# Optimization experiments

Hardware: AMD Instinct MI355X
Metric: run time of the kernel (lower is better)

## Reference

```python
import jax, jax.numpy as jnp
import numpy as np

ALPHA = 0.5            # conf['alpha'] hybrid mixing
MAX_TOP_ANT = 50       # conf['max_top_antecedents']
MAX_SPAN_WIDTH = 30


def bucket_distance(d):
    # util.bucket_distance: identity 0..4, then log2 buckets, clipped to [0, 9]
    logspace = jnp.floor(jnp.log2(jnp.maximum(d, 1).astype(jnp.float32))).astype(d.dtype) + 3
    return jnp.clip(jnp.where(d <= 4, d, logspace), 0, 9)


def setup_inputs() -> dict:
    key = jax.random.key(0)
    ks = jax.random.split(key, 16)
    W, D, K, F, H = 4096, 768, 768, 20, 1000
    SPAN = 3 * D                      # span_emb_size = 3 * bert_emb_size
    PAIR = 3 * SPAN + F               # pair_emb_size (use_features only)
    std = 0.02

    mention_doc = jax.random.normal(ks[0], (W, D), jnp.float32)
    mention_doc_one = jax.random.normal(ks[1], (W, D), jnp.float32)
    top_span_starts = jnp.sort(jax.random.randint(ks[2], (K,), 0, W - MAX_SPAN_WIDTH))
    widths = jax.random.randint(ks[3], (K,), 0, MAX_SPAN_WIDTH)
    top_span_ends = jnp.minimum(top_span_starts + widths, W - 1)
    top_span_mention_scores = jax.random.normal(ks[4], (K,), jnp.float32)

    return {
        "mention_doc": mention_doc,
        "mention_doc_one": mention_doc_one,
        "top_span_starts": top_span_starts,
        "top_span_ends": top_span_ends,
        "top_span_mention_scores": top_span_mention_scores,
        # mention_token_attn: Linear(D -> 1)
        "attn_w": jax.random.normal(ks[5], (D,), jnp.float32) * std,
        "attn_b": jnp.zeros((), jnp.float32),
        # coarse_bilinear: Linear(SPAN -> SPAN)
        "coarse_w": jax.random.normal(ks[6], (SPAN, SPAN), jnp.float32) * std,
        "coarse_b": jnp.zeros((SPAN,), jnp.float32),
        # emb_antecedent_distance_prior [10, F] + antecedent_distance_score_ffnn Linear(F -> 1)
        "dist_prior_emb": jax.random.normal(ks[7], (10, F), jnp.float32) * std,
        "dist_w": jax.random.normal(ks[8], (F,), jnp.float32) * std,
        "dist_b": jnp.zeros((), jnp.float32),
        # emb_top_antecedent_distance [10, F]
        "top_dist_emb": jax.random.normal(ks[9], (10, F), jnp.float32) * std,
        # coref_score_ffnn: Linear(PAIR -> H), ReLU, Linear(H -> 1)
        "coref_w1": jax.random.normal(ks[10], (PAIR, H), jnp.float32) * std,
        "coref_b1": jnp.zeros((H,), jnp.float32),
        "coref_w2": jax.random.normal(ks[11], (H,), jnp.float32) * std,
        "coref_b2": jnp.zeros((), jnp.float32),
    }


def reference(mention_doc, mention_doc_one, top_span_starts, top_span_ends,
              top_span_mention_scores, attn_w, attn_b, coarse_w, coarse_b,
              dist_prior_emb, dist_w, dist_b, top_dist_emb,
              coref_w1, coref_b1, coref_w2, coref_b2):
    W = mention_doc.shape[0]
    K = top_span_starts.shape[0]
    C = min(K, MAX_TOP_ANT)
    NEG_INF = jnp.float32(-1e30) * 0 - jnp.inf  # true -inf, matches torch.log(0.)

    # --- span embeddings: start / end / head-attention over hybrid doc ---
    start_emb = mention_doc[top_span_starts]                      # [K, D]
    end_emb = mention_doc[top_span_ends]                          # [K, D]
    hybrid = mention_doc * (1.0 - ALPHA) + mention_doc_one * ALPHA
    token_attn = hybrid @ attn_w + attn_b                         # [W]
    tok = jnp.arange(W)
    span_tok_mask = (tok[None, :] >= top_span_starts[:, None]) & \
                    (tok[None, :] <= top_span_ends[:, None])      # [K, W]
    attn_raw = jnp.where(span_tok_mask, token_attn[None, :], NEG_INF)
    attn_probs = jax.nn.softmax(attn_raw, axis=1)                 # [K, W]
    head_emb = attn_probs @ hybrid                                # [K, D]
    span_emb = jnp.concatenate([start_emb, end_emb, head_emb], axis=1)  # [K, 3D]

    # --- coarse (fast) pairwise scores ---
    rng = jnp.arange(K)
    ant_offsets = rng[:, None] - rng[None, :]                     # [K, K]
    ant_mask = ant_offsets >= 1
    pair_sum = top_span_mention_scores[:, None] + top_span_mention_scores[None, :]
    src = span_emb @ coarse_w + coarse_b                          # coarse_bilinear
    fast = pair_sum + src @ span_emb.T
    fast = jnp.where(ant_mask, fast, NEG_INF)                     # + log(mask)
    dist_score = dist_prior_emb @ dist_w + dist_b                 # [10]
    fast = fast + dist_score[bucket_distance(ant_offsets)]        # distance prior

    # --- top-k antecedent pruning ---
    top_fast, top_idx = jax.lax.top_k(fast, C)                    # [K, C]
    top_ant_offsets = jnp.take_along_axis(ant_offsets, top_idx, axis=1)

    # --- fine-grained pairwise FFNN scoring ---
    dist_emb = top_dist_emb[bucket_distance(top_ant_offsets)]     # [K, C, F]
    ant_emb = span_emb[top_idx]                                   # [K, C, 3D]
    tgt_emb = jnp.broadcast_to(span_emb[:, None, :], ant_emb.shape)
    sim_emb = span_emb[:, None, :] * ant_emb
    pair_emb = jnp.concatenate([tgt_emb, ant_emb, sim_emb, dist_emb], axis=-1)  # [K, C, PAIR]
    h = jax.nn.relu(jnp.einsum('kcp,ph->kch', pair_emb, coref_w1) + coref_b1)
    slow = jnp.einsum('kch,h->kc', h, coref_w2) + coref_b2        # [K, C]
    top_scores = slow + top_fast

    # dummy antecedent (epsilon) column of zeros
    return jnp.concatenate([jnp.zeros((K, 1), top_scores.dtype), top_scores], axis=1)
```

## Files before the change

### kernel.cpp

```cpp
#include <hip/hip_runtime.h>
#include <math.h>

#define WTOK 4096
#define DD   768
#define KK   768
#define SPAN 2304
#define HH   1000
#define CC   50
#define NPAD 1024
#define NBIG 4352

typedef __attribute__((ext_vector_type(8))) short bf16x8;
typedef __attribute__((ext_vector_type(4))) float f32x4;
typedef unsigned short ushort;
typedef unsigned int uint;

__device__ __forceinline__ int bucketd(int d) {
  int l = (d >= 1) ? (31 - __clz(d)) : 0;
  int v = (d <= 4) ? d : (l + 3);
  return min(max(v, 0), 9);
}
__device__ __forceinline__ ushort f2bf(float f) {
  uint u = __float_as_uint(f);
  return (ushort)((u + 0x7fffu + ((u >> 16) & 1u)) >> 16);
}
__device__ __forceinline__ uint pkmul_t(uint a, uint b) {
  float lo = __uint_as_float(a << 16) * __uint_as_float(b << 16);
  float hi = __uint_as_float(a & 0xffff0000u) * __uint_as_float(b & 0xffff0000u);
  return (__float_as_uint(lo) >> 16) | (__float_as_uint(hi) & 0xffff0000u);
}
__device__ __forceinline__ uint4 pkmul4(uint4 a, uint4 b) {
  uint4 r;
  r.x = pkmul_t(a.x, b.x); r.y = pkmul_t(a.y, b.y);
  r.z = pkmul_t(a.z, b.z); r.w = pkmul_t(a.w, b.w);
  return r;
}
__device__ __forceinline__ void dma16(const ushort* g, ushort* l) {
  __builtin_amdgcn_global_load_lds(
      (const __attribute__((address_space(1))) void*)g,
      (__attribute__((address_space(3))) void*)l, 16, 0, 0);
}

#define PB_COARSE 5184
#define PB_W 2304
#define PB_SETUP_BASE (PB_COARSE + 3 * PB_W)
#define PB_SLOW_BASE  (PB_SETUP_BASE + 40)
#define PB_TOTAL      (PB_SLOW_BASE + 150)

__global__ __launch_bounds__(256) void prep_k(
    const float* __restrict__ coarse_w, const float* __restrict__ W1,
    const float* __restrict__ dist_prior, const float* __restrict__ dist_w,
    const float* __restrict__ dist_b, const float* __restrict__ top_dist,
    ushort* __restrict__ BigT, ushort* __restrict__ W1simT,
    float* __restrict__ dist_score, float* __restrict__ Pdist,
    float* __restrict__ slow)
{
  int bid = blockIdx.x;
  int tid = threadIdx.x;
  if (bid >= PB_SLOW_BASE) {
    int t = (bid - PB_SLOW_BASE) * 256 + tid;
    if (t < KK * CC) slow[t] = 0.f;
    return;
  }
  if (bid >= PB_SETUP_BASE) {
    int t = (bid - PB_SETUP_BASE) * 256 + tid;
    if (t < 10) {
      float s = dist_b[0];
      for (int f = 0; f < 20; ++f) s += dist_prior[t * 20 + f] * dist_w[f];
      dist_score[t] = s;
    }
    if (t < 10 * HH) {
      int b = t / HH, h = t % HH;
      float s = 0.f;
      for (int f = 0; f < 20; ++f)
        s += top_dist[b * 20 + f] * W1[(long)(6912 + f) * HH + h];
      Pdist[t] = s;
    }
    return;
  }
  const float* in; int ldin, Cin, nbase, NBrows; ushort* out; int idx;
  int xt;
  if (bid < PB_COARSE) {
    idx = bid; in = coarse_w; ldin = SPAN; Cin = SPAN; nbase = 0;
    NBrows = NBIG; out = BigT; xt = SPAN / 32;
  } else {
    idx = bid - PB_COARSE;
    int region = idx / PB_W;
    idx = idx % PB_W;
    if (region == 0) { in = W1; nbase = 2304; NBrows = NBIG; out = BigT; }
    else if (region == 1) { in = W1 + (size_t)SPAN * HH; nbase = 3328; NBrows = NBIG; out = BigT; }
    else { in = W1 + (size_t)2 * SPAN * HH; nbase = 0; NBrows = NPAD; out = W1simT; }
    ldin = HH; Cin = HH; xt = NPAD / 32;
  }
  {
    int bx = idx % xt, by = idx / xt;
    __shared__ float tile[32][33];
    int n0 = bx * 32, p0 = by * 32;
    int tx = tid & 31, ty = tid >> 5;
    for (int i = ty; i < 32; i += 8) {
      int p = p0 + i, n = n0 + tx;
      tile[i][tx] = (n < Cin) ? in[(long)p * ldin + n] : 0.f;
    }
    __syncthreads();
    size_t slab = (size_t)(p0 >> 5) * NBrows * 32;
    for (int i = ty; i < 32; i += 8) {
      int n = n0 + i;
      out[slab + (size_t)(nbase + n) * 32 + tx] = f2bf(tile[tx][i]);
    }
  }
}

__global__ __launch_bounds__(256) void hybrid_attn_k(
    const float* __restrict__ doc, const float* __restrict__ doc1,
    const float* __restrict__ attn_w, const float* __restrict__ attn_b,
    float* __restrict__ hybrid, float* __restrict__ tok_attn)
{
  int w = blockIdx.x;
  int tid = threadIdx.x;
  float part = 0.f;
  for (int d = tid; d < DD; d += 256) {
    float h = 0.5f * doc[(long)w * DD + d] + 0.5f * doc1[(long)w * DD + d];
    hybrid[(long)w * DD + d] = h;
    part += h * attn_w[d];
  }
  for (int off = 32; off > 0; off >>= 1) part += __shfl_down(part, off, 64);
  __shared__ float ws4[4];
  if ((tid & 63) == 0) ws4[tid >> 6] = part;
  __syncthreads();
  if (tid == 0) tok_attn[w] = ws4[0] + ws4[1] + ws4[2] + ws4[3] + attn_b[0];
}

__global__ __launch_bounds__(256) void span_emb_k(
    const float* __restrict__ doc, const float* __restrict__ hybrid,
    const float* __restrict__ tok_attn, const int* __restrict__ starts,
    const int* __restrict__ ends, ushort* __restrict__ se_bf)
{
  int k = blockIdx.x;
  int s = starts[k], e = ends[k];
  int len = e - s + 1;
  int tid = threadIdx.x;
  __shared__ float p_s[32];
  if (tid < 32) {
    float v = (tid < len) ? tok_attn[s + tid] : -INFINITY;
    float m = v;
    for (int msk = 16; msk >= 1; msk >>= 1) m = fmaxf(m, __shfl_xor(m, msk, 32));
    float pe = (tid < len) ? expf(v - m) : 0.f;
    float Z = pe;
    for (int msk = 16; msk >= 1; msk >>= 1) Z += __shfl_xor(Z, msk, 32);
    p_s[tid] = pe / Z;
  }
  __syncthreads();
  for (int d = tid; d < DD; d += 256) {
    float h = 0.f;
    for (int t = 0; t < len; ++t) h += p_s[t] * hybrid[(long)(s + t) * DD + d];
    se_bf[(long)k * SPAN + d]          = f2bf(doc[(long)s * DD + d]);
    se_bf[(long)k * SPAN + DD + d]     = f2bf(doc[(long)e * DD + d]);
    se_bf[(long)k * SPAN + 2 * DD + d] = f2bf(h);
  }
}

__global__ __launch_bounds__(256) void gemm_combined_k(
    const ushort* __restrict__ A, const ushort* __restrict__ B,
    const float* __restrict__ coarse_b, const float* __restrict__ b1,
    ushort* __restrict__ src_bf, float* __restrict__ Ptgt,
    float* __restrict__ Pant)
{
  __shared__ __align__(16) ushort As[64 * 40];
  __shared__ __align__(16) ushort Bs[128 * 32];
  int tid = threadIdx.x;
  int m0 = blockIdx.x * 64, n0 = blockIdx.y * 128;
  int lane = tid & 63, wid = tid >> 6;
  int quad = lane >> 4, lr = lane & 15;
  int wm = (wid & 1) << 5, wn = (wid >> 1) << 6;
  int arow = tid >> 2, aq = tid & 3;
  int gofs[2];
#pragma unroll
  for (int t = 0; t < 2; ++t) {
    int S = t * 256 + tid;
    int r = S >> 2, p = S & 3;
    int q = p ^ ((r >> 1) & 3);
    gofs[t] = (n0 + r) * 32 + q * 8;
  }
  f32x4 acc[2][4] = {};
  for (int k0 = 0; k0 < SPAN; k0 += 32) {
    uint4 a0 = *(const uint4*)(A + (size_t)(m0 + arow) * SPAN + k0 + aq * 8);
    __syncthreads();
    const ushort* sb = B + (size_t)(k0 >> 5) * (NBIG * 32);
    dma16(sb + gofs[0], &Bs[(size_t)(0 * 256 + tid) * 8]);
    dma16(sb + gofs[1], &Bs[(size_t)(1 * 256 + tid) * 8]);
    *(uint4*)&As[arow * 40 + aq * 8] = a0;
    __syncthreads();
    bf16x8 af[2], bfr[4];
#pragma unroll
    for (int mi = 0; mi < 2; ++mi)
      af[mi] = *(const bf16x8*)&As[(wm + mi * 16 + lr) * 40 + quad * 8];
#pragma unroll
    for (int ni = 0; ni < 4; ++ni) {
      int r = wn + ni * 16 + lr;
      int p = quad ^ ((r >> 1) & 3);
      bfr[ni] = *(const bf16x8*)&Bs[r * 32 + p * 8];
    }
#pragma unroll
    for (int mi = 0; mi < 2; ++mi)
#pragma unroll
      for (int ni = 0; ni < 4; ++ni)
        acc[mi][ni] = __builtin_amdgcn_mfma_f32_16x16x32_bf16(
            af[mi], bfr[ni], acc[mi][ni], 0, 0, 0);
  }
#pragma unroll
  for (int mi = 0; mi < 2; ++mi)
#pragma unroll
    for (int ni = 0; ni < 4; ++ni) {
      f32x4 c = acc[mi][ni];
#pragma unroll
      for (int reg = 0; reg < 4; ++reg) {
        int gm = m0 + wm + mi * 16 + quad * 4 + reg;
        int g = n0 + wn + ni * 16 + lr;
        float v = c[reg];
        if (g < 2304) {
          src_bf[(size_t)gm * SPAN + g] = f2bf(v + coarse_b[g]);
        } else if (g < 3328) {
          int n = g - 2304;
          if (n < HH) Ptgt[(size_t)gm * HH + n] = v + b1[n];
        } else {
          int n = g - 3328;
          if (n < HH) Pant[(size_t)gm * HH + n] = v;
        }
      }
    }
}

__global__ __launch_bounds__(256) void gemm_fast_k(
    const ushort* __restrict__ A, const ushort* __restrict__ B,
    const float* __restrict__ ms, const float* __restrict__ dist_score,
    float* __restrict__ fast)
{
  __shared__ __align__(16) ushort As[64 * 40];
  __shared__ __align__(16) ushort Bs[64 * 40];
  int tid = threadIdx.x;
  int m0 = blockIdx.x * 64, n0 = blockIdx.y * 64;
  int lane = tid & 63, wid = tid >> 6;
  int quad = lane >> 4, lr = lane & 15;
  int wm = (wid & 1) << 5, wn = (wid >> 1) << 5;
  int row = tid >> 2, aq = tid & 3;
  const ushort* ga = A + (size_t)(m0 + row) * SPAN + aq * 8;
  const ushort* gb = B + (size_t)(n0 + row) * SPAN + aq * 8;
  f32x4 acc[2][2] = {};
  for (int k0 = 0; k0 < SPAN; k0 += 32) {
    uint4 a0 = *(const uint4*)(ga + k0);
    uint4 b0 = *(const uint4*)(gb + k0);
    __syncthreads();
    *(uint4*)&As[row * 40 + aq * 8] = a0;
    *(uint4*)&Bs[row * 40 + aq * 8] = b0;
    __syncthreads();
    bf16x8 af[2], bfr[2];
#pragma unroll
    for (int mi = 0; mi < 2; ++mi)
      af[mi] = *(const bf16x8*)&As[(wm + mi * 16 + lr) * 40 + quad * 8];
#pragma unroll
    for (int ni = 0; ni < 2; ++ni)
      bfr[ni] = *(const bf16x8*)&Bs[(wn + ni * 16 + lr) * 40 + quad * 8];
#pragma unroll
    for (int mi = 0; mi < 2; ++mi)
#pragma unroll
      for (int ni = 0; ni < 2; ++ni)
        acc[mi][ni] = __builtin_amdgcn_mfma_f32_16x16x32_bf16(
            af[mi], bfr[ni], acc[mi][ni], 0, 0, 0);
  }
#pragma unroll
  for (int mi = 0; mi < 2; ++mi)
#pragma unroll
    for (int ni = 0; ni < 2; ++ni) {
      f32x4 c = acc[mi][ni];
#pragma unroll
      for (int reg = 0; reg < 4; ++reg) {
        int gm = m0 + wm + mi * 16 + quad * 4 + reg;
        int gn = n0 + wn + ni * 16 + lr;
        float v;
        if (gn < gm) {
          v = c[reg] + ms[gm] + ms[gn] + dist_score[bucketd(gm - gn)];
        } else {
          v = -INFINITY;
        }
        fast[(size_t)gm * KK + gn] = v;
      }
    }
}

__global__ __launch_bounds__(256) void topk_k(
    const float* __restrict__ fast, float* __restrict__ top_fast,
    int* __restrict__ row_j, int* __restrict__ row_bucket)
{
  __shared__ float vals[KK];
  __shared__ float wbv[4];
  __shared__ int wbi[4];
  int k = blockIdx.x;
  int tid = threadIdx.x;
  for (int j = tid; j < KK; j += 256) vals[j] = fast[(long)k * KK + j];
  __syncthreads();
  const float NANF = __uint_as_float(0x7fc00000u);
  for (int it = 0; it < CC; ++it) {
    float bv = -INFINITY;
    int bi = 1 << 30;
    for (int j = tid; j < KK; j += 256) {
      float v = vals[j];
      if (v > bv || (v == bv && j < bi)) { bv = v; bi = j; }
    }
    for (int off = 32; off > 0; off >>= 1) {
      float ov = __shfl_down(bv, off, 64);
      int oi = __shfl_down(bi, off, 64);
      if (ov > bv || (ov == bv && oi < bi)) { bv = ov; bi = oi; }
    }
    if ((tid & 63) == 0) { wbv[tid >> 6] = bv; wbi[tid >> 6] = bi; }
    __syncthreads();
    if (tid == 0) {
      for (int w = 1; w < 4; ++w) {
        float ov = wbv[w]; int oi = wbi[w];
        if (ov > bv || (ov == bv && oi < bi)) { bv = ov; bi = oi; }
      }
      int r = k * CC + it;
      top_fast[r] = bv;
      row_j[r] = bi;
      row_bucket[r] = bucketd(k - bi);
      vals[bi] = NANF;
    }
    __syncthreads();
  }
}

__global__ __launch_bounds__(256, 4) void pair_mfma_k(
    const ushort* __restrict__ se_bf, const ushort* __restrict__ W1simT,
    const int* __restrict__ row_j, const int* __restrict__ row_bucket,
    const float* __restrict__ Ptgt, const float* __restrict__ Pant,
    const float* __restrict__ Pdist, const float* __restrict__ w2,
    float* __restrict__ slow)
{
  __shared__ __align__(16) ushort As[2][128 * 40];
  __shared__ __align__(16) ushort Bs[2][128 * 32];
  __shared__ int ks_s[128];
  __shared__ int js_s[128];
  __shared__ int bk_s[128];
  int tid = threadIdx.x;
  int m0 = blockIdx.x * 128, n0 = blockIdx.y * 128;
  if (tid < 128) {
    int r = m0 + tid;
    ks_s[tid] = r / CC;
    js_s[tid] = row_j[r];
    bk_s[tid] = row_bucket[r];
  }
  __syncthreads();
  int lane = tid & 63, wid = tid >> 6;
  int quad = lane >> 4, lr = lane & 15;
  int wm = (wid & 1) << 6, wn = (wid >> 1) << 6;
  int ar0 = tid >> 2, aq = tid & 3;
  const ushort* pk0 = se_bf + (size_t)ks_s[ar0] * SPAN + aq * 8;
  const ushort* pj0 = se_bf + (size_t)js_s[ar0] * SPAN + aq * 8;
  const ushort* pk1 = se_bf + (size_t)ks_s[ar0 + 64] * SPAN + aq * 8;
  const ushort* pj1 = se_bf + (size_t)js_s[ar0 + 64] * SPAN + aq * 8;
  int gofs[2];
#pragma unroll
  for (int t = 0; t < 2; ++t) {
    int S = t * 256 + tid;
    int r = S >> 2, p = S & 3;
    int q = p ^ ((r >> 1) & 3);
    gofs[t] = (n0 + r) * 32 + q * 8;
  }

  {
    uint4 ka0 = *(const uint4*)(pk0);
    uint4 ja0 = *(const uint4*)(pj0);
    uint4 ka1 = *(const uint4*)(pk1);
    uint4 ja1 = *(const uint4*)(pj1);
#pragma unroll
    for (int t = 0; t < 2; ++t)
      dma16(W1simT + gofs[t], &Bs[0][(size_t)(t * 256 + tid) * 8]);
    *(uint4*)&As[0][ar0 * 40 + aq * 8]        = pkmul4(ka0, ja0);
    *(uint4*)&As[0][(ar0 + 64) * 40 + aq * 8] = pkmul4(ka1, ja1);
  }
  __syncthreads();

  f32x4 acc[4][4] = {};
  for (int k0 = 0; k0 < SPAN; k0 += 32) {
    int buf = (k0 >> 5) & 1, nb = buf ^ 1;
    bool more = (k0 + 32) < SPAN;
    int k1 = more ? k0 + 32 : k0;
    uint4 ka0 = *(const uint4*)(pk0 + k1);
    uint4 ja0 = *(const uint4*)(pj0 + k1);
    uint4 ka1 = *(const uint4*)(pk1 + k1);
    uint4 ja1 = *(const uint4*)(pj1 + k1);
    if (more) {
      const ushort* sb = W1simT + (size_t)(k1 >> 5) * (NPAD * 32);
#pragma unroll
      for (int t = 0; t < 2; ++t)
        dma16(sb + gofs[t], &Bs[nb][(size_t)(t * 256 + tid) * 8]);
    }
    bf16x8 af[4], bfr[4];
#pragma unroll
    for (int mi = 0; mi < 4; ++mi)
      af[mi] = *(const bf16x8*)&As[buf][(wm + mi * 16 + lr) * 40 + quad * 8];
#pragma unroll
    for (int ni = 0; ni < 4; ++ni) {
      int r = wn + ni * 16 + lr;
      int p = quad ^ ((r >> 1) & 3);
      bfr[ni] = *(const bf16x8*)&Bs[buf][r * 32 + p * 8];
    }
#pragma unroll
    for (int ni = 0; ni < 4; ++ni)
#pragma unroll
      for (int mi = 0; mi < 4; ++mi)
        acc[mi][ni] = __builtin_amdgcn_mfma_f32_16x16x32_bf16(
            af[mi], bfr[ni], acc[mi][ni], 0, 0, 0);
    if (more) {
      *(uint4*)&As[nb][ar0 * 40 + aq * 8]        = pkmul4(ka0, ja0);
      *(uint4*)&As[nb][(ar0 + 64) * 40 + aq * 8] = pkmul4(ka1, ja1);
    }
    __syncthreads();
  }
  int nn[4]; float w2r[4]; bool nv[4];
#pragma unroll
  for (int ni = 0; ni < 4; ++ni) {
    nn[ni] = n0 + wn + ni * 16 + lr;
    nv[ni] = nn[ni] < HH;
    w2r[ni] = nv[ni] ? w2[nn[ni]] : 0.f;
  }
#pragma unroll
  for (int mi = 0; mi < 4; ++mi) {
#pragma unroll
    for (int reg = 0; reg < 4; ++reg) {
      int rl = wm + mi * 16 + quad * 4 + reg;
      int kk = ks_s[rl], jj = js_s[rl], bb = bk_s[rl];
      float s = 0.f;
#pragma unroll
      for (int ni = 0; ni < 4; ++ni) {
        if (nv[ni]) {
          float h = acc[mi][ni][reg] + Ptgt[(size_t)kk * HH + nn[ni]] +
                    Pant[(size_t)jj * HH + nn[ni]] +
                    Pdist[(size_t)bb * HH + nn[ni]];
          s += fmaxf(h, 0.f) * w2r[ni];
        }
      }
      s += __shfl_xor(s, 1); s += __shfl_xor(s, 2);
      s += __shfl_xor(s, 4); s += __shfl_xor(s, 8);
      if (lr == 0) atomicAdd(&slow[m0 + rl], s);
    }
  }
}

__global__ void finalize_k(const float* __restrict__ slow,
                           const float* __restrict__ top_fast,
                           const float* __restrict__ b2, float* __restrict__ out)
{
  int t = blockIdx.x * 256 + threadIdx.x;
  if (t >= KK * (CC + 1)) return;
  int k = t / (CC + 1), col = t % (CC + 1);
  if (col == 0) {
    out[t] = 0.f;
  } else {
    int r = k * CC + col - 1;
    float v = slow[r] + b2[0] + top_fast[r];
    if (!isfinite(v)) v = -1.0e30f;
    out[t] = v;
  }
}

extern "C" void kernel_launch(void* const* d_in, const int* in_sizes, int n_in,
                              void* d_out, int out_size, void* d_ws, size_t ws_size,
                              hipStream_t stream)
{
  const float* doc        = (const float*)d_in[0];
  const float* doc1       = (const float*)d_in[1];
  const int*   starts     = (const int*)d_in[2];
  const int*   ends       = (const int*)d_in[3];
  const float* ms         = (const float*)d_in[4];
  const float* attn_w     = (const float*)d_in[5];
  const float* attn_b     = (const float*)d_in[6];
  const float* coarse_w   = (const float*)d_in[7];
  const float* coarse_b   = (const float*)d_in[8];
  const float* dist_prior = (const float*)d_in[9];
  const float* dist_w     = (const float*)d_in[10];
  const float* dist_b     = (const float*)d_in[11];
  const float* top_dist   = (const float*)d_in[12];
  const float* W1         = (const float*)d_in[13];
  const float* b1         = (const float*)d_in[14];
  const float* w2         = (const float*)d_in[15];
  const float* b2         = (const float*)d_in[16];
  float* out = (float*)d_out;

  char* ws = (char*)d_ws;
  size_t off = 0;
  auto alloc = [&](size_t bytes) { void* p = ws + off; off = (off + bytes + 1023) & ~(size_t)1023; return p; };
  float*  hybrid     = (float*)alloc((size_t)WTOK * DD * 4);
  float*  tok_attn   = (float*)alloc((size_t)WTOK * 4);
  ushort* se_bf      = (ushort*)alloc((size_t)KK * SPAN * 2 + 4096);
  ushort* src_bf     = (ushort*)alloc((size_t)KK * SPAN * 2 + 4096);
  float*  fast       = (float*)alloc((size_t)KK * KK * 4);
  float*  Ptgt       = (float*)alloc((size_t)KK * HH * 4);
  float*  Pant       = (float*)alloc((size_t)KK * HH * 4);
  float*  Pdist      = (float*)alloc((size_t)10 * HH * 4);
  float*  dist_score = (float*)alloc(64);
  float*  top_fast   = (float*)alloc((size_t)KK * CC * 4);
  int*    row_j      = (int*)alloc((size_t)KK * CC * 4);
  int*    row_bucket = (int*)alloc((size_t)KK * CC * 4);
  float*  slow       = (float*)alloc((size_t)KK * CC * 4);
  ushort* BigT       = (ushort*)alloc((size_t)NBIG * SPAN * 2 + 4096);
  ushort* W1simT     = (ushort*)alloc((size_t)NPAD * SPAN * 2 + 4096);
  (void)ws_size; (void)in_sizes; (void)n_in; (void)out_size;

  prep_k<<<PB_TOTAL, 256, 0, stream>>>(coarse_w, W1, dist_prior, dist_w,
                                       dist_b, top_dist, BigT, W1simT,
                                       dist_score, Pdist, slow);
  hybrid_attn_k<<<WTOK, 256, 0, stream>>>(doc, doc1, attn_w, attn_b, hybrid, tok_attn);
  span_emb_k<<<KK, 256, 0, stream>>>(doc, hybrid, tok_attn, starts, ends, se_bf);
  {
    dim3 g(KK / 64, NBIG / 128);
    gemm_combined_k<<<g, 256, 0, stream>>>(se_bf, BigT, coarse_b, b1,
                                           src_bf, Ptgt, Pant);
  }
  {
    dim3 g(KK / 64, KK / 64);
    gemm_fast_k<<<g, 256, 0, stream>>>(src_bf, se_bf, ms, dist_score, fast);
  }
  topk_k<<<KK, 256, 0, stream>>>(fast, top_fast, row_j, row_bucket);
  {
    dim3 g((KK * CC) / 128, NPAD / 128);
    pair_mfma_k<<<g, 256, 0, stream>>>(se_bf, W1simT, row_j, row_bucket,
                                       Ptgt, Pant, Pdist, w2, slow);
  }
  finalize_k<<<(KK * (CC + 1) + 255) / 256, 256, 0, stream>>>(slow, top_fast, b2, out);
}
```

Baseline: 554.7 us.

## Precompute pairwise product matrix in a separate kernel and DMA it into the GEMM

Adds a prod_k kernel that writes the elementwise product of target and antecedent span embeddings into a k-slab-major bf16 buffer (about 177 MB), overlaid on workspace that is dead by then. The pair GEMM then loads the A tile with async DMA and a swizzled LDS layout, the same way as the B tile, instead of doing two gathered global loads and a multiply per step. Blocks are remapped so the eight N tiles that share an M tile are spread across the launch order. The aim is to take gather latency and VALU work out of the MFMA loop, at the cost of an extra large write and read through HBM.

```diff
diff --git a/kernel.cpp b/kernel.cpp
--- a/kernel.cpp
+++ b/kernel.cpp
@@ -9,6 +9,8 @@
 #define CC   50
 #define NPAD 1024
 #define NBIG 4352
+#define PROWS (KK * CC)
+#define PCHUNK (PROWS * 4)
 
 typedef __attribute__((ext_vector_type(8))) short bf16x8;
 typedef __attribute__((ext_vector_type(4))) float f32x4;
@@ -328,54 +330,62 @@
   }
 }
 
+__global__ __launch_bounds__(256) void prod_k(
+    const ushort* __restrict__ se_bf, const int* __restrict__ row_j,
+    ushort* __restrict__ AsimT)
+{
+  int u = blockIdx.x * 256 + threadIdx.x;
+  int c = u / PCHUNK;
+  int rem = u - c * PCHUNK;
+  int r = rem >> 2;
+  int q = rem & 3;
+  int kidx = r / CC;
+  int j = row_j[r];
+  int koff = c * 32 + q * 8;
+  uint4 a = *(const uint4*)(se_bf + (size_t)kidx * SPAN + koff);
+  uint4 b = *(const uint4*)(se_bf + (size_t)j * SPAN + koff);
+  *(uint4*)(AsimT + (size_t)c * ((size_t)PROWS * 32) + (size_t)r * 32 + q * 8) =
+      pkmul4(a, b);
+}
+
 __global__ __launch_bounds__(256, 4) void pair_mfma_k(
-    const ushort* __restrict__ se_bf, const ushort* __restrict__ W1simT,
+    const ushort* __restrict__ AsimT, const ushort* __restrict__ W1simT,
     const int* __restrict__ row_j, const int* __restrict__ row_bucket,
     const float* __restrict__ Ptgt, const float* __restrict__ Pant,
     const float* __restrict__ Pdist, const float* __restrict__ w2,
     float* __restrict__ slow)
 {
-  __shared__ __align__(16) ushort As[2][128 * 40];
+  __shared__ __align__(16) ushort As[2][128 * 32];
   __shared__ __align__(16) ushort Bs[2][128 * 32];
   __shared__ int ks_s[128];
   __shared__ int js_s[128];
   __shared__ int bk_s[128];
   int tid = threadIdx.x;
-  int m0 = blockIdx.x * 128, n0 = blockIdx.y * 128;
+  int b = blockIdx.x;
+  int t = (b & 7) * 300 + (b >> 3);
+  int m0 = (t >> 3) * 128, n0 = (t & 7) * 128;
   if (tid < 128) {
     int r = m0 + tid;
     ks_s[tid] = r / CC;
     js_s[tid] = row_j[r];
     bk_s[tid] = row_bucket[r];
   }
-  __syncthreads();
   int lane = tid & 63, wid = tid >> 6;
   int quad = lane >> 4, lr = lane & 15;
   int wm = (wid & 1) << 6, wn = (wid >> 1) << 6;
-  int ar0 = tid >> 2, aq = tid & 3;
-  const ushort* pk0 = se_bf + (size_t)ks_s[ar0] * SPAN + aq * 8;
-  const ushort* pj0 = se_bf + (size_t)js_s[ar0] * SPAN + aq * 8;
-  const ushort* pk1 = se_bf + (size_t)ks_s[ar0 + 64] * SPAN + aq * 8;
-  const ushort* pj1 = se_bf + (size_t)js_s[ar0 + 64] * SPAN + aq * 8;
-  int gofs[2];
-#pragma unroll
-  for (int t = 0; t < 2; ++t) {
-    int S = t * 256 + tid;
+  int aofs[2], bofs[2];
+#pragma unroll
+  for (int tt = 0; tt < 2; ++tt) {
+    int S = tt * 256 + tid;
     int r = S >> 2, p = S & 3;
     int q = p ^ ((r >> 1) & 3);
-    gofs[t] = (n0 + r) * 32 + q * 8;
-  }
-
-  {
-    uint4 ka0 = *(const uint4*)(pk0);
-    uint4 ja0 = *(const uint4*)(pj0);
-    uint4 ka1 = *(const uint4*)(pk1);
-    uint4 ja1 = *(const uint4*)(pj1);
-#pragma unroll
-    for (int t = 0; t < 2; ++t)
-      dma16(W1simT + gofs[t], &Bs[0][(size_t)(t * 256 + tid) * 8]);
-    *(uint4*)&As[0][ar0 * 40 + aq * 8]        = pkmul4(ka0, ja0);
-    *(uint4*)&As[0][(ar0 + 64) * 40 + aq * 8] = pkmul4(ka1, ja1);
+    aofs[tt] = (m0 + r) * 32 + q * 8;
+    bofs[tt] = (n0 + r) * 32 + q * 8;
+  }
+#pragma unroll
+  for (int tt = 0; tt < 2; ++tt) {
+    dma16(AsimT + aofs[tt],  &As[0][(size_t)(tt * 256 + tid) * 8]);
+    dma16(W1simT + bofs[tt], &Bs[0][(size_t)(tt * 256 + tid) * 8]);
   }
   __syncthreads();
 
@@ -383,21 +393,23 @@
   for (int k0 = 0; k0 < SPAN; k0 += 32) {
     int buf = (k0 >> 5) & 1, nb = buf ^ 1;
     bool more = (k0 + 32) < SPAN;
-    int k1 = more ? k0 + 32 : k0;
-    uint4 ka0 = *(const uint4*)(pk0 + k1);
-    uint4 ja0 = *(const uint4*)(pj0 + k1);
-    uint4 ka1 = *(const uint4*)(pk1 + k1);
-    uint4 ja1 = *(const uint4*)(pj1 + k1);
     if (more) {
-      const ushort* sb = W1simT + (size_t)(k1 >> 5) * (NPAD * 32);
-#pragma unroll
-      for (int t = 0; t < 2; ++t)
-        dma16(sb + gofs[t], &Bs[nb][(size_t)(t * 256 + tid) * 8]);
+      size_t slab = (size_t)((k0 >> 5) + 1);
+#pragma unroll
+      for (int tt = 0; tt < 2; ++tt) {
+        dma16(AsimT + slab * ((size_t)PROWS * 32) + aofs[tt],
+              &As[nb][(size_t)(tt * 256 + tid) * 8]);
+        dma16(W1simT + slab * (NPAD * 32) + bofs[tt],
+              &Bs[nb][(size_t)(tt * 256 + tid) * 8]);
+      }
     }
     bf16x8 af[4], bfr[4];
 #pragma unroll
-    for (int mi = 0; mi < 4; ++mi)
-      af[mi] = *(const bf16x8*)&As[buf][(wm + mi * 16 + lr) * 40 + quad * 8];
+    for (int mi = 0; mi < 4; ++mi) {
+      int r = wm + mi * 16 + lr;
+      int p = quad ^ ((r >> 1) & 3);
+      af[mi] = *(const bf16x8*)&As[buf][r * 32 + p * 8];
+    }
 #pragma unroll
     for (int ni = 0; ni < 4; ++ni) {
       int r = wn + ni * 16 + lr;
@@ -410,10 +422,6 @@
       for (int mi = 0; mi < 4; ++mi)
         acc[mi][ni] = __builtin_amdgcn_mfma_f32_16x16x32_bf16(
             af[mi], bfr[ni], acc[mi][ni], 0, 0, 0);
-    if (more) {
-      *(uint4*)&As[nb][ar0 * 40 + aq * 8]        = pkmul4(ka0, ja0);
-      *(uint4*)&As[nb][(ar0 + 64) * 40 + aq * 8] = pkmul4(ka1, ja1);
-    }
     __syncthreads();
   }
   int nn[4]; float w2r[4]; bool nv[4];
@@ -489,11 +497,7 @@
   char* ws = (char*)d_ws;
   size_t off = 0;
   auto alloc = [&](size_t bytes) { void* p = ws + off; off = (off + bytes + 1023) & ~(size_t)1023; return p; };
-  float*  hybrid     = (float*)alloc((size_t)WTOK * DD * 4);
-  float*  tok_attn   = (float*)alloc((size_t)WTOK * 4);
   ushort* se_bf      = (ushort*)alloc((size_t)KK * SPAN * 2 + 4096);
-  ushort* src_bf     = (ushort*)alloc((size_t)KK * SPAN * 2 + 4096);
-  float*  fast       = (float*)alloc((size_t)KK * KK * 4);
   float*  Ptgt       = (float*)alloc((size_t)KK * HH * 4);
   float*  Pant       = (float*)alloc((size_t)KK * HH * 4);
   float*  Pdist      = (float*)alloc((size_t)10 * HH * 4);
@@ -502,8 +506,14 @@
   int*    row_j      = (int*)alloc((size_t)KK * CC * 4);
   int*    row_bucket = (int*)alloc((size_t)KK * CC * 4);
   float*  slow       = (float*)alloc((size_t)KK * CC * 4);
+  ushort* W1simT     = (ushort*)alloc((size_t)NPAD * SPAN * 2 + 4096);
+  size_t ovl = off;
+  float*  hybrid     = (float*)alloc((size_t)WTOK * DD * 4);
+  float*  tok_attn   = (float*)alloc((size_t)WTOK * 4);
+  ushort* src_bf     = (ushort*)alloc((size_t)KK * SPAN * 2 + 4096);
+  float*  fast       = (float*)alloc((size_t)KK * KK * 4);
   ushort* BigT       = (ushort*)alloc((size_t)NBIG * SPAN * 2 + 4096);
-  ushort* W1simT     = (ushort*)alloc((size_t)NPAD * SPAN * 2 + 4096);
+  ushort* AsimT      = (ushort*)(ws + ovl);
   (void)ws_size; (void)in_sizes; (void)n_in; (void)out_size;
 
   prep_k<<<PB_TOTAL, 256, 0, stream>>>(coarse_w, W1, dist_prior, dist_w,
@@ -521,10 +531,8 @@
     gemm_fast_k<<<g, 256, 0, stream>>>(src_bf, se_bf, ms, dist_score, fast);
   }
   topk_k<<<KK, 256, 0, stream>>>(fast, top_fast, row_j, row_bucket);
-  {
-    dim3 g((KK * CC) / 128, NPAD / 128);
-    pair_mfma_k<<<g, 256, 0, stream>>>(se_bf, W1simT, row_j, row_bucket,
-                                       Ptgt, Pant, Pdist, w2, slow);
-  }
+  prod_k<<<(72 * PCHUNK) / 256, 256, 0, stream>>>(se_bf, row_j, AsimT);
+  pair_mfma_k<<<(PROWS / 128) * (NPAD / 128), 256, 0, stream>>>(
+      AsimT, W1simT, row_j, row_bucket, Ptgt, Pant, Pdist, w2, slow);
   finalize_k<<<(KK * (CC + 1) + 255) / 256, 256, 0, stream>>>(slow, top_fast, b2, out);
 }
```

Result: slower. 580.4 us (+4.6%).
